# Kernel optimization log

Hardware: AMD Instinct MI355X
Metric: run time of the kernel (lower is better)

Reference implementation:

```python
import jax, jax.numpy as jnp
import numpy as np

HID = 32
R = 3
B = 2
IN = 64
N = 100000
E = 1600000
G = 256


def setup_inputs() -> dict:
    key = jax.random.key(0)
    ks = jax.random.split(key, 16)
    x = jax.random.normal(ks[0], (N, IN), dtype=jnp.float32)
    src = jax.random.randint(ks[1], (E,), 0, N)
    dst = jax.random.randint(ks[2], (E,), 0, N)
    etype = jax.random.randint(ks[3], (E,), 0, R)
    graph_ids = jnp.sort(jax.random.randint(ks[4], (N,), 0, G))
    s = 0.05
    basis1 = jax.random.normal(ks[5], (B, IN, HID), dtype=jnp.float32) * s   # layer 1 basis
    basis_r = jax.random.normal(ks[6], (3, B, HID, HID), dtype=jnp.float32) * s  # layers 2-4
    w_comp = jax.random.normal(ks[7], (4, R, B), dtype=jnp.float32) * s     # per-layer basis coeffs
    loop1 = jax.random.normal(ks[8], (IN, HID), dtype=jnp.float32) * s
    loop_r = jax.random.normal(ks[9], (3, HID, HID), dtype=jnp.float32) * s
    bias = jnp.zeros((4, HID), dtype=jnp.float32)
    lin1_w = jax.random.normal(ks[10], (4 * HID, 64), dtype=jnp.float32) * s
    lin1_b = jnp.zeros((64,), dtype=jnp.float32)
    lin2_w = jax.random.normal(ks[11], (64, 1), dtype=jnp.float32) * s
    lin2_b = jnp.zeros((1,), dtype=jnp.float32)
    return dict(x=x, basis1=basis1, basis_r=basis_r, w_comp=w_comp, loop1=loop1,
                loop_r=loop_r, bias=bias, lin1_w=lin1_w, lin1_b=lin1_b,
                lin2_w=lin2_w, lin2_b=lin2_b, src=src, dst=dst, etype=etype,
                graph_ids=graph_ids, num_graphs=G)


def _rel_conv(h, basis, comp, loop_w, b, src, dst, etype, n_nodes):
    # basis-decomposed relation weights: W[r] = sum_b comp[r,b] * basis[b]
    W = jnp.einsum('rb,bio->rio', comp, basis)            # [R, in, out]
    h_rel = jnp.einsum('ni,rio->rno', h, W)               # [R, N, out]
    msg = h_rel[etype, src]                               # [E, out] edge-typed gather
    agg = jax.ops.segment_sum(msg, dst, num_segments=n_nodes)
    return agg + h @ loop_w + b                           # self-loop + bias


def reference(x, basis1, basis_r, w_comp, loop1, loop_r, bias,
              lin1_w, lin1_b, lin2_w, lin2_b,
              src, dst, etype, graph_ids, num_graphs):
    n = x.shape[0]
    h = jnp.tanh(_rel_conv(x, basis1, w_comp[0], loop1, bias[0], src, dst, etype, n))
    states = [h]
    for i in range(3):
        h = jnp.tanh(_rel_conv(h, basis_r[i], w_comp[i + 1], loop_r[i], bias[i + 1],
                               src, dst, etype, n))
        states.append(h)
    feat = jnp.concatenate(states, axis=1)                # [N, 128]
    # mean-pool nodes per graph (diff_pooling ~ dgl mean_nodes)
    summed = jax.ops.segment_sum(feat, graph_ids, num_segments=num_graphs)
    counts = jax.ops.segment_sum(jnp.ones((n,), feat.dtype), graph_ids,
                                 num_segments=num_graphs)
    pooled = summed / jnp.maximum(counts, 1.0)[:, None]   # [G, 128]
    hdn = jax.nn.relu(pooled @ lin1_w + lin1_b)
    out = jax.nn.sigmoid(hdn @ lin2_w + lin2_b)
    return out[:, 0]
```

## Files before the change

kernel.cpp:

```cpp
#include <hip/hip_runtime.h>
#include <cstdint>
#include <cmath>

#define DLO_BITS 7
#define DLO_MASK 127
#define SCAT_Q 2048

__global__ __launch_bounds__(256) void count_kernel(
    const int* __restrict__ dst, int* __restrict__ bcnt, int E, int NB)
{
    __shared__ int cnt[1024];
    for (int i = threadIdx.x; i < NB; i += 256) cnt[i] = 0;
    __syncthreads();
    int base = blockIdx.x * SCAT_Q;
    #pragma unroll
    for (int i = 0; i < SCAT_Q / 256; ++i) {
        int e = base + i * 256 + threadIdx.x;
        if (e < E) atomicAdd(&cnt[dst[e] >> DLO_BITS], 1);
    }
    __syncthreads();
    for (int i = threadIdx.x; i < NB; i += 256)
        if (cnt[i]) atomicAdd(&bcnt[i], cnt[i]);
}

__global__ __launch_bounds__(1024) void scan_kernel(
    const int* __restrict__ bcnt, int* __restrict__ bbase,
    int* __restrict__ bcur, int NB)
{
    __shared__ int s[1024];
    int t = threadIdx.x;
    int v = (t < NB) ? bcnt[t] : 0;
    s[t] = v; __syncthreads();
    for (int off = 1; off < 1024; off <<= 1) {
        int u = (t >= off) ? s[t - off] : 0;
        __syncthreads();
        s[t] += u;
        __syncthreads();
    }
    if (t < NB) { int b = s[t] - v; bbase[t] = b; bcur[t] = b; }
}

__global__ __launch_bounds__(256) void bscatter_kernel(
    const int* __restrict__ src, const int* __restrict__ dst,
    const int* __restrict__ et, int* __restrict__ bcur,
    unsigned* __restrict__ eidx1, int E, int NB)
{
    __shared__ int cnt[1024];
    __shared__ int bbs[1024];
    int tid = threadIdx.x;
    for (int i = tid; i < NB; i += 256) cnt[i] = 0;
    __syncthreads();
    int base = blockIdx.x * SCAT_Q;
    int lim = E - base; if (lim > SCAT_Q) lim = SCAT_Q;
    for (int i = tid; i < lim; i += 256)
        atomicAdd(&cnt[dst[base + i] >> DLO_BITS], 1);
    __syncthreads();
    for (int i = tid; i < NB; i += 256) {
        int c = cnt[i];
        bbs[i] = c ? atomicAdd(&bcur[i], c) : 0;
    }
    __syncthreads();
    for (int i = tid; i < NB; i += 256) cnt[i] = 0;
    __syncthreads();
    for (int i = tid; i < lim; i += 256) {
        int e = base + i;
        int d = dst[e];
        int bk = d >> DLO_BITS;
        int p = bbs[bk] + atomicAdd(&cnt[bk], 1);
        eidx1[p] = (unsigned)src[e] | ((unsigned)et[e] << 17)
                 | ((unsigned)(d & DLO_MASK) << 19);
    }
}

__global__ __launch_bounds__(256) void bucket_sort_kernel(
    const unsigned* __restrict__ eidx1, const int* __restrict__ bbase,
    const int* __restrict__ bcnt, unsigned* __restrict__ eidx2,
    int* __restrict__ rp, int* __restrict__ rend, int N)
{
    __shared__ int c128[128], excl[128], w[128];
    int tid = threadIdx.x, b = blockIdx.x;
    int gbase = bbase[b], cnt = bcnt[b], n0 = b << DLO_BITS;
    if (tid < 128) c128[tid] = 0;
    __syncthreads();
    for (int k = tid; k < cnt; k += 256)
        atomicAdd(&c128[(eidx1[gbase + k] >> 19) & DLO_MASK], 1);
    __syncthreads();
    if (tid < 128) w[tid] = c128[tid];
    __syncthreads();
    for (int off = 1; off < 128; off <<= 1) {
        int u = (tid < 128 && tid >= off) ? w[tid - off] : 0;
        __syncthreads();
        if (tid < 128) w[tid] += u;
        __syncthreads();
    }
    if (tid < 128) {
        excl[tid] = w[tid] - c128[tid];
        int n = n0 + tid;
        if (n < N) { rp[n] = gbase + excl[tid]; rend[n] = gbase + excl[tid] + c128[tid]; }
        c128[tid] = 0;
    }
    __syncthreads();
    for (int k = tid; k < cnt; k += 256) {
        unsigned pk = eidx1[gbase + k];
        int dlo = (pk >> 19) & DLO_MASK;
        int p = excl[dlo] + atomicAdd(&c128[dlo], 1);
        eidx2[gbase + p] = pk;
    }
}

__global__ __launch_bounds__(256) void dense_kernel(
    const float* __restrict__ x,
    const float* __restrict__ basis1,
    const float* __restrict__ loop1,
    const float* __restrict__ w_comp,
    const float* __restrict__ bias_l,
    float* __restrict__ hrel,
    float* __restrict__ agg,
    int N)
{
    __shared__ float sW[4 * 2048];
    __shared__ float sH[64 * 68];
    const int tid = threadIdx.x;
    for (int i = tid; i < 4 * 2048; i += 256) {
        int m = i >> 11, io = i & 2047;
        float v;
        if (m < 3) v = w_comp[m * 2] * basis1[io] + w_comp[m * 2 + 1] * basis1[2048 + io];
        else       v = loop1[io];
        sW[i] = v;
    }
    const int nb = blockIdx.x * 64;
    for (int idx = tid; idx < 64 * 64; idx += 256) {
        int n = idx >> 6, i = idx & 63;
        int gn = nb + n;
        sH[n * 68 + i] = (gn < N) ? x[(size_t)gn * 64 + i] : 0.0f;
    }
    __syncthreads();

    const int m  = tid >> 6;
    const int l  = tid & 63;
    const int ow = l & 7;
    const int ng = l >> 3;

    float acc[8][4];
    #pragma unroll
    for (int j = 0; j < 8; ++j)
        #pragma unroll
        for (int k = 0; k < 4; ++k) acc[j][k] = 0.0f;

    const float* wb = &sW[m * 2048 + ow * 4];
    #pragma unroll 2
    for (int i = 0; i < 64; i += 4) {
        float4 wv0 = *(const float4*)(wb + (i + 0) * 32);
        float4 wv1 = *(const float4*)(wb + (i + 1) * 32);
        float4 wv2 = *(const float4*)(wb + (i + 2) * 32);
        float4 wv3 = *(const float4*)(wb + (i + 3) * 32);
        #pragma unroll
        for (int j = 0; j < 8; ++j) {
            float4 hv = *(const float4*)&sH[(j * 8 + ng) * 68 + i];
            acc[j][0] += hv.x * wv0.x + hv.y * wv1.x + hv.z * wv2.x + hv.w * wv3.x;
            acc[j][1] += hv.x * wv0.y + hv.y * wv1.y + hv.z * wv2.y + hv.w * wv3.y;
            acc[j][2] += hv.x * wv0.z + hv.y * wv1.z + hv.z * wv2.z + hv.w * wv3.z;
            acc[j][3] += hv.x * wv0.w + hv.y * wv1.w + hv.z * wv2.w + hv.w * wv3.w;
        }
    }

    if (m < 3) {
        #pragma unroll
        for (int j = 0; j < 8; ++j) {
            int n = nb + j * 8 + ng;
            if (n < N)
                *(float4*)&hrel[((size_t)m * N + n) * 32 + ow * 4] =
                    make_float4(acc[j][0], acc[j][1], acc[j][2], acc[j][3]);
        }
    } else {
        float4 bb = *(const float4*)&bias_l[ow * 4];
        #pragma unroll
        for (int j = 0; j < 8; ++j) {
            int n = nb + j * 8 + ng;
            if (n < N)
                *(float4*)&agg[(size_t)n * 32 + ow * 4] =
                    make_float4(acc[j][0] + bb.x, acc[j][1] + bb.y,
                                acc[j][2] + bb.z, acc[j][3] + bb.w);
        }
    }
}

__global__ __launch_bounds__(256) void gather1_kernel(
    const unsigned* __restrict__ eidx, const int* __restrict__ rp,
    const int* __restrict__ rend, const float* __restrict__ hrel,
    const float* __restrict__ agg, float* __restrict__ feat, int N)
{
    int tid = blockIdx.x * 256 + threadIdx.x;
    int n = tid >> 3;
    if (n >= N) return;
    int c = (tid & 7) << 2;
    int base = rp[n], cnt = rend[n] - base;
    const float4 bv = *(const float4*)&agg[(size_t)n * 32 + c];
    float a0[4] = {bv.x, bv.y, bv.z, bv.w};
    float a1[4] = {0, 0, 0, 0}, a2[4] = {0, 0, 0, 0}, a3[4] = {0, 0, 0, 0};
    int k = 0;
    for (; k + 4 <= cnt; k += 4) {
        unsigned p0 = eidx[base + k + 0], p1 = eidx[base + k + 1];
        unsigned p2 = eidx[base + k + 2], p3 = eidx[base + k + 3];
        float4 v0 = *(const float4*)&hrel[(((size_t)((p0 >> 17) & 3)) * N + (p0 & 0x1FFFF)) * 32 + c];
        float4 v1 = *(const float4*)&hrel[(((size_t)((p1 >> 17) & 3)) * N + (p1 & 0x1FFFF)) * 32 + c];
        float4 v2 = *(const float4*)&hrel[(((size_t)((p2 >> 17) & 3)) * N + (p2 & 0x1FFFF)) * 32 + c];
        float4 v3 = *(const float4*)&hrel[(((size_t)((p3 >> 17) & 3)) * N + (p3 & 0x1FFFF)) * 32 + c];
        a0[0] += v0.x; a0[1] += v0.y; a0[2] += v0.z; a0[3] += v0.w;
        a1[0] += v1.x; a1[1] += v1.y; a1[2] += v1.z; a1[3] += v1.w;
        a2[0] += v2.x; a2[1] += v2.y; a2[2] += v2.z; a2[3] += v2.w;
        a3[0] += v3.x; a3[1] += v3.y; a3[2] += v3.z; a3[3] += v3.w;
    }
    for (; k < cnt; ++k) {
        unsigned p = eidx[base + k];
        float4 v = *(const float4*)&hrel[(((size_t)((p >> 17) & 3)) * N + (p & 0x1FFFF)) * 32 + c];
        a0[0] += v.x; a0[1] += v.y; a0[2] += v.z; a0[3] += v.w;
    }
    float r0 = a0[0] + a1[0] + a2[0] + a3[0];
    float r1 = a0[1] + a1[1] + a2[1] + a3[1];
    float r2 = a0[2] + a1[2] + a2[2] + a3[2];
    float r3 = a0[3] + a1[3] + a2[3] + a3[3];
    float4* out = (float4*)&feat[(size_t)n * 128 + c];
    *out = make_float4(tanhf(r0), tanhf(r1), tanhf(r2), tanhf(r3));
}

__global__ __launch_bounds__(256) void fused_layer_kernel(
    const unsigned* __restrict__ eidx, const int* __restrict__ rp,
    const int* __restrict__ rend,
    const float* __restrict__ basis_b,
    const float* __restrict__ loop_w,
    const float* __restrict__ bias_l,
    const float* __restrict__ comp,
    const float* __restrict__ feat_in,
    float* __restrict__ feat_out,
    int N)
{
    __shared__ float sB0[1024], sB1[1024], sL[1024];
    __shared__ float sT0[32 * 36], sT1[32 * 36], sH[32 * 36];
    const int tid = threadIdx.x;
    for (int i = tid; i < 1024; i += 256) {
        sB0[i] = basis_b[i];
        sB1[i] = basis_b[1024 + i];
        sL[i]  = loop_w[i];
    }
    const float cc0r0 = comp[0], cc1r0 = comp[1];
    const float cc0r1 = comp[2], cc1r1 = comp[3];
    const float cc0r2 = comp[4], cc1r2 = comp[5];

    const int nn = tid >> 3, cg = (tid & 7) << 2;
    const int n = blockIdx.x * 32 + nn;

    float4 h4 = *(const float4*)&feat_in[(size_t)n * 128 + cg];
    *(float4*)&sH[nn * 36 + cg] = h4;

    const int base = rp[n], cnt = rend[n] - base;
    float t0a[4] = {0,0,0,0}, t1a[4] = {0,0,0,0};
    float t0b[4] = {0,0,0,0}, t1b[4] = {0,0,0,0};
    int k = 0;
    for (; k + 4 <= cnt; k += 4) {
        unsigned p0 = eidx[base + k + 0], p1 = eidx[base + k + 1];
        unsigned p2 = eidx[base + k + 2], p3 = eidx[base + k + 3];
        int r0 = (p0 >> 17) & 3, r1 = (p1 >> 17) & 3;
        int r2 = (p2 >> 17) & 3, r3 = (p3 >> 17) & 3;
        float4 v0 = *(const float4*)&feat_in[(size_t)(p0 & 0x1FFFF) * 128 + cg];
        float4 v1 = *(const float4*)&feat_in[(size_t)(p1 & 0x1FFFF) * 128 + cg];
        float4 v2 = *(const float4*)&feat_in[(size_t)(p2 & 0x1FFFF) * 128 + cg];
        float4 v3 = *(const float4*)&feat_in[(size_t)(p3 & 0x1FFFF) * 128 + cg];
        float c00 = r0 == 0 ? cc0r0 : (r0 == 1 ? cc0r1 : cc0r2);
        float c10 = r0 == 0 ? cc1r0 : (r0 == 1 ? cc1r1 : cc1r2);
        float c01 = r1 == 0 ? cc0r0 : (r1 == 1 ? cc0r1 : cc0r2);
        float c11 = r1 == 0 ? cc1r0 : (r1 == 1 ? cc1r1 : cc1r2);
        float c02 = r2 == 0 ? cc0r0 : (r2 == 1 ? cc0r1 : cc0r2);
        float c12 = r2 == 0 ? cc1r0 : (r2 == 1 ? cc1r1 : cc1r2);
        float c03 = r3 == 0 ? cc0r0 : (r3 == 1 ? cc0r1 : cc0r2);
        float c13 = r3 == 0 ? cc1r0 : (r3 == 1 ? cc1r1 : cc1r2);
        t0a[0] += c00*v0.x; t0a[1] += c00*v0.y; t0a[2] += c00*v0.z; t0a[3] += c00*v0.w;
        t1a[0] += c10*v0.x; t1a[1] += c10*v0.y; t1a[2] += c10*v0.z; t1a[3] += c10*v0.w;
        t0b[0] += c01*v1.x; t0b[1] += c01*v1.y; t0b[2] += c01*v1.z; t0b[3] += c01*v1.w;
        t1b[0] += c11*v1.x; t1b[1] += c11*v1.y; t1b[2] += c11*v1.z; t1b[3] += c11*v1.w;
        t0a[0] += c02*v2.x; t0a[1] += c02*v2.y; t0a[2] += c02*v2.z; t0a[3] += c02*v2.w;
        t1a[0] += c12*v2.x; t1a[1] += c12*v2.y; t1a[2] += c12*v2.z; t1a[3] += c12*v2.w;
        t0b[0] += c03*v3.x; t0b[1] += c03*v3.y; t0b[2] += c03*v3.z; t0b[3] += c03*v3.w;
        t1b[0] += c13*v3.x; t1b[1] += c13*v3.y; t1b[2] += c13*v3.z; t1b[3] += c13*v3.w;
    }
    for (; k < cnt; ++k) {
        unsigned p = eidx[base + k];
        int r = (p >> 17) & 3;
        float4 v = *(const float4*)&feat_in[(size_t)(p & 0x1FFFF) * 128 + cg];
        float c0 = r == 0 ? cc0r0 : (r == 1 ? cc0r1 : cc0r2);
        float c1 = r == 0 ? cc1r0 : (r == 1 ? cc1r1 : cc1r2);
        t0a[0] += c0*v.x; t0a[1] += c0*v.y; t0a[2] += c0*v.z; t0a[3] += c0*v.w;
        t1a[0] += c1*v.x; t1a[1] += c1*v.y; t1a[2] += c1*v.z; t1a[3] += c1*v.w;
    }
    *(float4*)&sT0[nn * 36 + cg] = make_float4(t0a[0]+t0b[0], t0a[1]+t0b[1],
                                               t0a[2]+t0b[2], t0a[3]+t0b[3]);
    *(float4*)&sT1[nn * 36 + cg] = make_float4(t1a[0]+t1b[0], t1a[1]+t1b[1],
                                               t1a[2]+t1b[2], t1a[3]+t1b[3]);
    __syncthreads();

    float4 bb = *(const float4*)&bias_l[cg];
    float a[4] = {bb.x, bb.y, bb.z, bb.w};
    #pragma unroll 8
    for (int kk = 0; kk < 32; ++kk) {
        float p0 = sT0[nn * 36 + kk];
        float p1 = sT1[nn * 36 + kk];
        float hh = sH[nn * 36 + kk];
        float4 b0 = *(const float4*)&sB0[kk * 32 + cg];
        float4 b1 = *(const float4*)&sB1[kk * 32 + cg];
        float4 lw = *(const float4*)&sL[kk * 32 + cg];
        a[0] += p0 * b0.x + p1 * b1.x + hh * lw.x;
        a[1] += p0 * b0.y + p1 * b1.y + hh * lw.y;
        a[2] += p0 * b0.z + p1 * b1.z + hh * lw.z;
        a[3] += p0 * b0.w + p1 * b1.w + hh * lw.w;
    }
    *(float4*)&feat_out[(size_t)n * 128 + cg] =
        make_float4(tanhf(a[0]), tanhf(a[1]), tanhf(a[2]), tanhf(a[3]));
}

__global__ __launch_bounds__(256) void pool_kernel(
    const float* __restrict__ feat, const int* __restrict__ gid,
    float* __restrict__ pooled, float* __restrict__ cntArr, int N)
{
    int chunk0 = blockIdx.x * 128;
    int ch = threadIdx.x & 127, half = threadIdx.x >> 7;
    int n = chunk0 + half;
    int lim = chunk0 + 128; if (lim > N) lim = N;
    if (n >= lim) return;
    int cur = gid[n];
    float acc = 0.0f; int cc = 0;
    for (; n < lim; n += 2) {
        int g = gid[n];
        if (g != cur) {
            atomicAdd(&pooled[(size_t)cur * 128 + ch], acc);
            if (ch == 0) atomicAdd(&cntArr[cur], (float)cc);
            acc = 0.0f; cc = 0; cur = g;
        }
        acc += feat[(size_t)n * 128 + ch];
        ++cc;
    }
    atomicAdd(&pooled[(size_t)cur * 128 + ch], acc);
    if (ch == 0) atomicAdd(&cntArr[cur], (float)cc);
}

__global__ __launch_bounds__(64) void mlp_kernel(
    const float* __restrict__ pooled, const float* __restrict__ cntArr,
    const float* __restrict__ w1, const float* __restrict__ b1,
    const float* __restrict__ w2, const float* __restrict__ b2,
    float* __restrict__ out)
{
    int g = blockIdx.x;
    int t = threadIdx.x;
    float inv = 1.0f / fmaxf(cntArr[g], 1.0f);
    float acc = b1[t];
    #pragma unroll 8
    for (int k = 0; k < 128; ++k)
        acc += pooled[(size_t)g * 128 + k] * inv * w1[k * 64 + t];
    float h = fmaxf(acc, 0.0f);
    float p = h * w2[t];
    #pragma unroll
    for (int off = 32; off > 0; off >>= 1) p += __shfl_down(p, off, 64);
    if (t == 0) out[g] = 1.0f / (1.0f + expf(-(p + b2[0])));
}

extern "C" void kernel_launch(void* const* d_in, const int* in_sizes, int n_in,
                              void* d_out, int out_size, void* d_ws, size_t ws_size,
                              hipStream_t stream)
{
    const float* x       = (const float*)d_in[0];
    const float* basis1  = (const float*)d_in[1];
    const float* basis_r = (const float*)d_in[2];
    const float* w_comp  = (const float*)d_in[3];
    const float* loop1   = (const float*)d_in[4];
    const float* loop_r  = (const float*)d_in[5];
    const float* bias    = (const float*)d_in[6];
    const float* lin1_w  = (const float*)d_in[7];
    const float* lin1_b  = (const float*)d_in[8];
    const float* lin2_w  = (const float*)d_in[9];
    const float* lin2_b  = (const float*)d_in[10];
    const int*   src     = (const int*)d_in[11];
    const int*   dst     = (const int*)d_in[12];
    const int*   etype   = (const int*)d_in[13];
    const int*   gid     = (const int*)d_in[14];

    const int N = in_sizes[0] / 64;
    const int E = in_sizes[11];
    const int G = out_size;
    const int NB = (N + DLO_MASK) >> DLO_BITS;

    float* ws      = (float*)d_ws;
    float* hrel    = ws;
    float* agg     = hrel + (size_t)3 * N * 32;
    float* feat    = agg + (size_t)N * 32;
    float* pooled  = feat + (size_t)N * 128;
    float* cntArr  = pooled + (size_t)G * 128;
    int*   bcnt    = (int*)(cntArr + G);
    int*   bbase   = bcnt + NB;
    int*   bcur    = bbase + NB;
    int*   rp      = bcur + NB;
    int*   rend    = rp + N;
    unsigned* eidx2 = (unsigned*)(rend + N);
    unsigned* eidx1 = (unsigned*)feat;

    hipMemsetAsync(pooled, 0, ((size_t)G * 128 + G + NB) * sizeof(float), stream);

    const int nsb = (E + SCAT_Q - 1) / SCAT_Q;
    count_kernel<<<nsb, 256, 0, stream>>>(dst, bcnt, E, NB);
    scan_kernel<<<1, 1024, 0, stream>>>(bcnt, bbase, bcur, NB);
    bscatter_kernel<<<nsb, 256, 0, stream>>>(src, dst, etype, bcur, eidx1, E, NB);
    bucket_sort_kernel<<<NB, 256, 0, stream>>>(eidx1, bbase, bcnt, eidx2, rp, rend, N);

    dense_kernel<<<(N + 63) / 64, 256, 0, stream>>>(x, basis1, loop1, w_comp, bias, hrel, agg, N);
    gather1_kernel<<<(N * 8 + 255) / 256, 256, 0, stream>>>(eidx2, rp, rend, hrel, agg, feat, N);

    for (int l = 1; l < 4; ++l) {
        fused_layer_kernel<<<(N + 31) / 32, 256, 0, stream>>>(
            eidx2, rp, rend,
            basis_r + (size_t)(l - 1) * 2048,
            loop_r + (size_t)(l - 1) * 1024,
            bias + l * 32,
            w_comp + l * 6,
            feat + (l - 1) * 32,
            feat + l * 32,
            N);
    }

    pool_kernel<<<(N + 127) / 128, 256, 0, stream>>>(feat, gid, pooled, cntArr, N);
    mlp_kernel<<<G, 64, 0, stream>>>(pooled, cntArr, lin1_w, lin1_b, lin2_w, lin2_b, (float*)d_out);
}
```

Before: 343.7 us.

## Precompute layer-1 relation weights once and read them as wave-uniform scalars in dense kernel

Adds a small prep kernel that builds the combined layer-1 relation and self-loop weights into workspace once, instead of every block rebuilding 32KB of weights in shared memory. The dense kernel is restructured so each wave takes one weight matrix (made wave-uniform with readfirstlane) and each lane computes all 32 outputs for one node, so the weight reads can become scalar loads. This cuts shared-memory use and per-block setup work. In exchange it needs 32 accumulators per lane, adds a kernel launch, and writes full 128-byte rows per lane, which are less coalesced stores.

```diff
diff --git a/kernel.cpp b/kernel.cpp
--- a/kernel.cpp
+++ b/kernel.cpp
@@ -5,6 +5,21 @@
 #define DLO_BITS 7
 #define DLO_MASK 127
 #define SCAT_Q 2048
+
+__global__ __launch_bounds__(256) void prep_w(
+    const float* __restrict__ basis1,
+    const float* __restrict__ w_comp,
+    const float* __restrict__ loop1,
+    float* __restrict__ W)
+{
+    int tid = blockIdx.x * 256 + threadIdx.x;
+    if (tid < 8192) {
+        int m = tid >> 11, io = tid & 2047;
+        W[tid] = (m < 3)
+            ? w_comp[m * 2] * basis1[io] + w_comp[m * 2 + 1] * basis1[2048 + io]
+            : loop1[io];
+    }
+}
 
 __global__ __launch_bounds__(256) void count_kernel(
     const int* __restrict__ dst, int* __restrict__ bcnt, int E, int NB)
@@ -110,24 +125,14 @@
 
 __global__ __launch_bounds__(256) void dense_kernel(
     const float* __restrict__ x,
-    const float* __restrict__ basis1,
-    const float* __restrict__ loop1,
-    const float* __restrict__ w_comp,
+    const float* __restrict__ W,
     const float* __restrict__ bias_l,
     float* __restrict__ hrel,
     float* __restrict__ agg,
     int N)
 {
-    __shared__ float sW[4 * 2048];
     __shared__ float sH[64 * 68];
     const int tid = threadIdx.x;
-    for (int i = tid; i < 4 * 2048; i += 256) {
-        int m = i >> 11, io = i & 2047;
-        float v;
-        if (m < 3) v = w_comp[m * 2] * basis1[io] + w_comp[m * 2 + 1] * basis1[2048 + io];
-        else       v = loop1[io];
-        sW[i] = v;
-    }
     const int nb = blockIdx.x * 64;
     for (int idx = tid; idx < 64 * 64; idx += 256) {
         int n = idx >> 6, i = idx & 63;
@@ -136,51 +141,37 @@
     }
     __syncthreads();
 
-    const int m  = tid >> 6;
-    const int l  = tid & 63;
-    const int ow = l & 7;
-    const int ng = l >> 3;
-
-    float acc[8][4];
+    const int m = __builtin_amdgcn_readfirstlane(tid >> 6);
+    const int l = tid & 63;
+    const float* wm = W + m * 2048;
+
+    float acc[32];
     #pragma unroll
-    for (int j = 0; j < 8; ++j)
+    for (int c = 0; c < 32; ++c) acc[c] = 0.0f;
+
+    #pragma unroll
+    for (int k0 = 0; k0 < 64; k0 += 4) {
+        float4 xv = *(const float4*)&sH[l * 68 + k0];
+        const float* w0 = wm + k0 * 32;
         #pragma unroll
-        for (int k = 0; k < 4; ++k) acc[j][k] = 0.0f;
-
-    const float* wb = &sW[m * 2048 + ow * 4];
-    #pragma unroll 2
-    for (int i = 0; i < 64; i += 4) {
-        float4 wv0 = *(const float4*)(wb + (i + 0) * 32);
-        float4 wv1 = *(const float4*)(wb + (i + 1) * 32);
-        float4 wv2 = *(const float4*)(wb + (i + 2) * 32);
-        float4 wv3 = *(const float4*)(wb + (i + 3) * 32);
-        #pragma unroll
-        for (int j = 0; j < 8; ++j) {
-            float4 hv = *(const float4*)&sH[(j * 8 + ng) * 68 + i];
-            acc[j][0] += hv.x * wv0.x + hv.y * wv1.x + hv.z * wv2.x + hv.w * wv3.x;
-            acc[j][1] += hv.x * wv0.y + hv.y * wv1.y + hv.z * wv2.y + hv.w * wv3.y;
-            acc[j][2] += hv.x * wv0.z + hv.y * wv1.z + hv.z * wv2.z + hv.w * wv3.z;
-            acc[j][3] += hv.x * wv0.w + hv.y * wv1.w + hv.z * wv2.w + hv.w * wv3.w;
-        }
-    }
-
-    if (m < 3) {
-        #pragma unroll
-        for (int j = 0; j < 8; ++j) {
-            int n = nb + j * 8 + ng;
-            if (n < N)
-                *(float4*)&hrel[((size_t)m * N + n) * 32 + ow * 4] =
-                    make_float4(acc[j][0], acc[j][1], acc[j][2], acc[j][3]);
-        }
-    } else {
-        float4 bb = *(const float4*)&bias_l[ow * 4];
-        #pragma unroll
-        for (int j = 0; j < 8; ++j) {
-            int n = nb + j * 8 + ng;
-            if (n < N)
-                *(float4*)&agg[(size_t)n * 32 + ow * 4] =
-                    make_float4(acc[j][0] + bb.x, acc[j][1] + bb.y,
-                                acc[j][2] + bb.z, acc[j][3] + bb.w);
+        for (int c = 0; c < 32; ++c)
+            acc[c] += xv.x * w0[c] + xv.y * w0[32 + c]
+                    + xv.z * w0[64 + c] + xv.w * w0[96 + c];
+    }
+
+    int n = nb + l;
+    if (n < N) {
+        if (m < 3) {
+            float* out = &hrel[((size_t)m * N + n) * 32];
+            #pragma unroll
+            for (int c = 0; c < 32; c += 4)
+                *(float4*)(out + c) = make_float4(acc[c], acc[c+1], acc[c+2], acc[c+3]);
+        } else {
+            float* out = &agg[(size_t)n * 32];
+            #pragma unroll
+            for (int c = 0; c < 32; c += 4)
+                *(float4*)(out + c) = make_float4(acc[c] + bias_l[c],   acc[c+1] + bias_l[c+1],
+                                                  acc[c+2] + bias_l[c+2], acc[c+3] + bias_l[c+3]);
         }
     }
 }
@@ -388,7 +379,8 @@
     const int NB = (N + DLO_MASK) >> DLO_BITS;
 
     float* ws      = (float*)d_ws;
-    float* hrel    = ws;
+    float* W       = ws;
+    float* hrel    = W + 8192;
     float* agg     = hrel + (size_t)3 * N * 32;
     float* feat    = agg + (size_t)N * 32;
     float* pooled  = feat + (size_t)N * 128;
@@ -402,6 +394,7 @@
     unsigned* eidx1 = (unsigned*)feat;
 
     hipMemsetAsync(pooled, 0, ((size_t)G * 128 + G + NB) * sizeof(float), stream);
+    prep_w<<<32, 256, 0, stream>>>(basis1, w_comp, loop1, W);
 
     const int nsb = (E + SCAT_Q - 1) / SCAT_Q;
     count_kernel<<<nsb, 256, 0, stream>>>(dst, bcnt, E, NB);
@@ -409,7 +402,7 @@
     bscatter_kernel<<<nsb, 256, 0, stream>>>(src, dst, etype, bcur, eidx1, E, NB);
     bucket_sort_kernel<<<NB, 256, 0, stream>>>(eidx1, bbase, bcnt, eidx2, rp, rend, N);
 
-    dense_kernel<<<(N + 63) / 64, 256, 0, stream>>>(x, basis1, loop1, w_comp, bias, hrel, agg, N);
+    dense_kernel<<<(N + 63) / 64, 256, 0, stream>>>(x, W, bias, hrel, agg, N);
     gather1_kernel<<<(N * 8 + 255) / 256, 256, 0, stream>>>(eidx2, rp, rend, hrel, agg, feat, N);
 
     for (int l = 1; l < 4; ++l) {
```

Measured after the change: 347.1 us. Within noise of the previous version (+1.0%).

## Sort edges by (dst, etype) to drop per-edge relation selects in gathers

Applied to the files above, without the earlier changes.

The bucket sort now keys on destination node and edge type together, producing three per-relation segment boundaries per node. Gather kernels loop over each relation segment separately, so the fused layers apply the basis coefficients once per segment instead of selecting and multiplying per edge, and layer 1 uses a fixed relation base pointer. The combined relation weights for layer 1 are also precomputed once in a small kernel instead of being rebuilt in every dense block. In exchange the sort scans 512 keys instead of 128, two extra offset arrays are written and read, and the split loops have shorter unrolled bodies with more tail handling.

```diff
diff --git a/kernel.cpp b/kernel.cpp
--- a/kernel.cpp
+++ b/kernel.cpp
@@ -5,6 +5,21 @@
 #define DLO_BITS 7
 #define DLO_MASK 127
 #define SCAT_Q 2048
+
+__global__ __launch_bounds__(256) void prep_w(
+    const float* __restrict__ basis1,
+    const float* __restrict__ w_comp,
+    const float* __restrict__ loop1,
+    float* __restrict__ W)
+{
+    int tid = blockIdx.x * 256 + threadIdx.x;
+    if (tid < 8192) {
+        int m = tid >> 11, io = tid & 2047;
+        W[tid] = (m < 3)
+            ? w_comp[m * 2] * basis1[io] + w_comp[m * 2 + 1] * basis1[2048 + io]
+            : loop1[io];
+    }
+}
 
 __global__ __launch_bounds__(256) void count_kernel(
     const int* __restrict__ dst, int* __restrict__ bcnt, int E, int NB)
@@ -75,44 +90,56 @@
 __global__ __launch_bounds__(256) void bucket_sort_kernel(
     const unsigned* __restrict__ eidx1, const int* __restrict__ bbase,
     const int* __restrict__ bcnt, unsigned* __restrict__ eidx2,
-    int* __restrict__ rp, int* __restrict__ rend, int N)
-{
-    __shared__ int c128[128], excl[128], w[128];
+    int* __restrict__ rp, int* __restrict__ rend0, int* __restrict__ rend1,
+    int* __restrict__ rend, int N)
+{
+    __shared__ int c512[512], excl[512], w[512];
     int tid = threadIdx.x, b = blockIdx.x;
     int gbase = bbase[b], cnt = bcnt[b], n0 = b << DLO_BITS;
-    if (tid < 128) c128[tid] = 0;
-    __syncthreads();
-    for (int k = tid; k < cnt; k += 256)
-        atomicAdd(&c128[(eidx1[gbase + k] >> 19) & DLO_MASK], 1);
-    __syncthreads();
-    if (tid < 128) w[tid] = c128[tid];
-    __syncthreads();
-    for (int off = 1; off < 128; off <<= 1) {
-        int u = (tid < 128 && tid >= off) ? w[tid - off] : 0;
-        __syncthreads();
-        if (tid < 128) w[tid] += u;
-        __syncthreads();
-    }
-    if (tid < 128) {
-        excl[tid] = w[tid] - c128[tid];
-        int n = n0 + tid;
-        if (n < N) { rp[n] = gbase + excl[tid]; rend[n] = gbase + excl[tid] + c128[tid]; }
-        c128[tid] = 0;
-    }
+    c512[tid] = 0; c512[tid + 256] = 0;
     __syncthreads();
     for (int k = tid; k < cnt; k += 256) {
         unsigned pk = eidx1[gbase + k];
-        int dlo = (pk >> 19) & DLO_MASK;
-        int p = excl[dlo] + atomicAdd(&c128[dlo], 1);
+        int key = (((pk >> 19) & DLO_MASK) << 2) | ((pk >> 17) & 3);
+        atomicAdd(&c512[key], 1);
+    }
+    __syncthreads();
+    w[tid] = c512[tid]; w[tid + 256] = c512[tid + 256];
+    __syncthreads();
+    for (int off = 1; off < 512; off <<= 1) {
+        int a1 = (tid >= off) ? w[tid - off] : 0;
+        int a2 = (tid + 256 >= off) ? w[tid + 256 - off] : 0;
+        __syncthreads();
+        w[tid] += a1; w[tid + 256] += a2;
+        __syncthreads();
+    }
+    excl[tid] = w[tid] - c512[tid];
+    excl[tid + 256] = w[tid + 256] - c512[tid + 256];
+    __syncthreads();
+    if (tid < 128) {
+        int n = n0 + tid;
+        if (n < N) {
+            int k0 = tid << 2;
+            rp[n]    = gbase + excl[k0];
+            rend0[n] = gbase + excl[k0 | 1];
+            rend1[n] = gbase + excl[k0 | 2];
+            rend[n]  = gbase + excl[k0 | 2] + c512[k0 | 2];
+        }
+    }
+    __syncthreads();
+    c512[tid] = 0; c512[tid + 256] = 0;
+    __syncthreads();
+    for (int k = tid; k < cnt; k += 256) {
+        unsigned pk = eidx1[gbase + k];
+        int key = (((pk >> 19) & DLO_MASK) << 2) | ((pk >> 17) & 3);
+        int p = excl[key] + atomicAdd(&c512[key], 1);
         eidx2[gbase + p] = pk;
     }
 }
 
 __global__ __launch_bounds__(256) void dense_kernel(
     const float* __restrict__ x,
-    const float* __restrict__ basis1,
-    const float* __restrict__ loop1,
-    const float* __restrict__ w_comp,
+    const float* __restrict__ W,
     const float* __restrict__ bias_l,
     float* __restrict__ hrel,
     float* __restrict__ agg,
@@ -121,13 +148,7 @@
     __shared__ float sW[4 * 2048];
     __shared__ float sH[64 * 68];
     const int tid = threadIdx.x;
-    for (int i = tid; i < 4 * 2048; i += 256) {
-        int m = i >> 11, io = i & 2047;
-        float v;
-        if (m < 3) v = w_comp[m * 2] * basis1[io] + w_comp[m * 2 + 1] * basis1[2048 + io];
-        else       v = loop1[io];
-        sW[i] = v;
-    }
+    for (int i = tid; i < 4 * 2048; i += 256) sW[i] = W[i];
     const int nb = blockIdx.x * 64;
     for (int idx = tid; idx < 64 * 64; idx += 256) {
         int n = idx >> 6, i = idx & 63;
@@ -187,45 +208,45 @@
 
 __global__ __launch_bounds__(256) void gather1_kernel(
     const unsigned* __restrict__ eidx, const int* __restrict__ rp,
-    const int* __restrict__ rend, const float* __restrict__ hrel,
-    const float* __restrict__ agg, float* __restrict__ feat, int N)
+    const int* __restrict__ rend0, const int* __restrict__ rend1,
+    const int* __restrict__ rend,
+    const float* __restrict__ hrel, const float* __restrict__ agg,
+    float* __restrict__ feat, int N)
 {
     int tid = blockIdx.x * 256 + threadIdx.x;
     int n = tid >> 3;
     if (n >= N) return;
     int c = (tid & 7) << 2;
-    int base = rp[n], cnt = rend[n] - base;
+    int e0 = rp[n], e1 = rend0[n], e2 = rend1[n], e3 = rend[n];
     const float4 bv = *(const float4*)&agg[(size_t)n * 32 + c];
-    float a0[4] = {bv.x, bv.y, bv.z, bv.w};
-    float a1[4] = {0, 0, 0, 0}, a2[4] = {0, 0, 0, 0}, a3[4] = {0, 0, 0, 0};
-    int k = 0;
-    for (; k + 4 <= cnt; k += 4) {
-        unsigned p0 = eidx[base + k + 0], p1 = eidx[base + k + 1];
-        unsigned p2 = eidx[base + k + 2], p3 = eidx[base + k + 3];
-        float4 v0 = *(const float4*)&hrel[(((size_t)((p0 >> 17) & 3)) * N + (p0 & 0x1FFFF)) * 32 + c];
-        float4 v1 = *(const float4*)&hrel[(((size_t)((p1 >> 17) & 3)) * N + (p1 & 0x1FFFF)) * 32 + c];
-        float4 v2 = *(const float4*)&hrel[(((size_t)((p2 >> 17) & 3)) * N + (p2 & 0x1FFFF)) * 32 + c];
-        float4 v3 = *(const float4*)&hrel[(((size_t)((p3 >> 17) & 3)) * N + (p3 & 0x1FFFF)) * 32 + c];
-        a0[0] += v0.x; a0[1] += v0.y; a0[2] += v0.z; a0[3] += v0.w;
-        a1[0] += v1.x; a1[1] += v1.y; a1[2] += v1.z; a1[3] += v1.w;
-        a2[0] += v2.x; a2[1] += v2.y; a2[2] += v2.z; a2[3] += v2.w;
-        a3[0] += v3.x; a3[1] += v3.y; a3[2] += v3.z; a3[3] += v3.w;
-    }
-    for (; k < cnt; ++k) {
-        unsigned p = eidx[base + k];
-        float4 v = *(const float4*)&hrel[(((size_t)((p >> 17) & 3)) * N + (p & 0x1FFFF)) * 32 + c];
-        a0[0] += v.x; a0[1] += v.y; a0[2] += v.z; a0[3] += v.w;
-    }
-    float r0 = a0[0] + a1[0] + a2[0] + a3[0];
-    float r1 = a0[1] + a1[1] + a2[1] + a3[1];
-    float r2 = a0[2] + a1[2] + a2[2] + a3[2];
-    float r3 = a0[3] + a1[3] + a2[3] + a3[3];
+    float ax = bv.x, ay = bv.y, az = bv.z, aw = bv.w;
+    float bx = 0, by = 0, bz = 0, bw = 0;
+    #pragma unroll
+    for (int seg = 0; seg < 3; ++seg) {
+        int ks = (seg == 0) ? e0 : ((seg == 1) ? e1 : e2);
+        int ke = (seg == 0) ? e1 : ((seg == 1) ? e2 : e3);
+        const float* hb = hrel + (size_t)seg * N * 32 + c;
+        int k = ks;
+        for (; k + 2 <= ke; k += 2) {
+            unsigned p0 = eidx[k], p1 = eidx[k + 1];
+            float4 v0 = *(const float4*)&hb[(size_t)(p0 & 0x1FFFF) * 32];
+            float4 v1 = *(const float4*)&hb[(size_t)(p1 & 0x1FFFF) * 32];
+            ax += v0.x; ay += v0.y; az += v0.z; aw += v0.w;
+            bx += v1.x; by += v1.y; bz += v1.z; bw += v1.w;
+        }
+        if (k < ke) {
+            unsigned p = eidx[k];
+            float4 v = *(const float4*)&hb[(size_t)(p & 0x1FFFF) * 32];
+            ax += v.x; ay += v.y; az += v.z; aw += v.w;
+        }
+    }
     float4* out = (float4*)&feat[(size_t)n * 128 + c];
-    *out = make_float4(tanhf(r0), tanhf(r1), tanhf(r2), tanhf(r3));
+    *out = make_float4(tanhf(ax + bx), tanhf(ay + by), tanhf(az + bz), tanhf(aw + bw));
 }
 
 __global__ __launch_bounds__(256) void fused_layer_kernel(
     const unsigned* __restrict__ eidx, const int* __restrict__ rp,
+    const int* __restrict__ rend0, const int* __restrict__ rend1,
     const int* __restrict__ rend,
     const float* __restrict__ basis_b,
     const float* __restrict__ loop_w,
@@ -243,59 +264,41 @@
         sB1[i] = basis_b[1024 + i];
         sL[i]  = loop_w[i];
     }
-    const float cc0r0 = comp[0], cc1r0 = comp[1];
-    const float cc0r1 = comp[2], cc1r1 = comp[3];
-    const float cc0r2 = comp[4], cc1r2 = comp[5];
-
     const int nn = tid >> 3, cg = (tid & 7) << 2;
     const int n = blockIdx.x * 32 + nn;
 
     float4 h4 = *(const float4*)&feat_in[(size_t)n * 128 + cg];
     *(float4*)&sH[nn * 36 + cg] = h4;
 
-    const int base = rp[n], cnt = rend[n] - base;
-    float t0a[4] = {0,0,0,0}, t1a[4] = {0,0,0,0};
-    float t0b[4] = {0,0,0,0}, t1b[4] = {0,0,0,0};
-    int k = 0;
-    for (; k + 4 <= cnt; k += 4) {
-        unsigned p0 = eidx[base + k + 0], p1 = eidx[base + k + 1];
-        unsigned p2 = eidx[base + k + 2], p3 = eidx[base + k + 3];
-        int r0 = (p0 >> 17) & 3, r1 = (p1 >> 17) & 3;
-        int r2 = (p2 >> 17) & 3, r3 = (p3 >> 17) & 3;
-        float4 v0 = *(const float4*)&feat_in[(size_t)(p0 & 0x1FFFF) * 128 + cg];
-        float4 v1 = *(const float4*)&feat_in[(size_t)(p1 & 0x1FFFF) * 128 + cg];
-        float4 v2 = *(const float4*)&feat_in[(size_t)(p2 & 0x1FFFF) * 128 + cg];
-        float4 v3 = *(const float4*)&feat_in[(size_t)(p3 & 0x1FFFF) * 128 + cg];
-        float c00 = r0 == 0 ? cc0r0 : (r0 == 1 ? cc0r1 : cc0r2);
-        float c10 = r0 == 0 ? cc1r0 : (r0 == 1 ? cc1r1 : cc1r2);
-        float c01 = r1 == 0 ? cc0r0 : (r1 == 1 ? cc0r1 : cc0r2);
-        float c11 = r1 == 0 ? cc1r0 : (r1 == 1 ? cc1r1 : cc1r2);
-        float c02 = r2 == 0 ? cc0r0 : (r2 == 1 ? cc0r1 : cc0r2);
-        float c12 = r2 == 0 ? cc1r0 : (r2 == 1 ? cc1r1 : cc1r2);
-        float c03 = r3 == 0 ? cc0r0 : (r3 == 1 ? cc0r1 : cc0r2);
-        float c13 = r3 == 0 ? cc1r0 : (r3 == 1 ? cc1r1 : cc1r2);
-        t0a[0] += c00*v0.x; t0a[1] += c00*v0.y; t0a[2] += c00*v0.z; t0a[3] += c00*v0.w;
-        t1a[0] += c10*v0.x; t1a[1] += c10*v0.y; t1a[2] += c10*v0.z; t1a[3] += c10*v0.w;
-        t0b[0] += c01*v1.x; t0b[1] += c01*v1.y; t0b[2] += c01*v1.z; t0b[3] += c01*v1.w;
-        t1b[0] += c11*v1.x; t1b[1] += c11*v1.y; t1b[2] += c11*v1.z; t1b[3] += c11*v1.w;
-        t0a[0] += c02*v2.x; t0a[1] += c02*v2.y; t0a[2] += c02*v2.z; t0a[3] += c02*v2.w;
-        t1a[0] += c12*v2.x; t1a[1] += c12*v2.y; t1a[2] += c12*v2.z; t1a[3] += c12*v2.w;
-        t0b[0] += c03*v3.x; t0b[1] += c03*v3.y; t0b[2] += c03*v3.z; t0b[3] += c03*v3.w;
-        t1b[0] += c13*v3.x; t1b[1] += c13*v3.y; t1b[2] += c13*v3.z; t1b[3] += c13*v3.w;
-    }
-    for (; k < cnt; ++k) {
-        unsigned p = eidx[base + k];
-        int r = (p >> 17) & 3;
-        float4 v = *(const float4*)&feat_in[(size_t)(p & 0x1FFFF) * 128 + cg];
-        float c0 = r == 0 ? cc0r0 : (r == 1 ? cc0r1 : cc0r2);
-        float c1 = r == 0 ? cc1r0 : (r == 1 ? cc1r1 : cc1r2);
-        t0a[0] += c0*v.x; t0a[1] += c0*v.y; t0a[2] += c0*v.z; t0a[3] += c0*v.w;
-        t1a[0] += c1*v.x; t1a[1] += c1*v.y; t1a[2] += c1*v.z; t1a[3] += c1*v.w;
-    }
-    *(float4*)&sT0[nn * 36 + cg] = make_float4(t0a[0]+t0b[0], t0a[1]+t0b[1],
-                                               t0a[2]+t0b[2], t0a[3]+t0b[3]);
-    *(float4*)&sT1[nn * 36 + cg] = make_float4(t1a[0]+t1b[0], t1a[1]+t1b[1],
-                                               t1a[2]+t1b[2], t1a[3]+t1b[3]);
+    int e0 = rp[n], e1 = rend0[n], e2 = rend1[n], e3 = rend[n];
+    float t0x = 0, t0y = 0, t0z = 0, t0w = 0;
+    float t1x = 0, t1y = 0, t1z = 0, t1w = 0;
+    #pragma unroll
+    for (int seg = 0; seg < 3; ++seg) {
+        int ks = (seg == 0) ? e0 : ((seg == 1) ? e1 : e2);
+        int ke = (seg == 0) ? e1 : ((seg == 1) ? e2 : e3);
+        float sx = 0, sy = 0, sz = 0, sw = 0;
+        float ux = 0, uy = 0, uz = 0, uw = 0;
+        int k = ks;
+        for (; k + 2 <= ke; k += 2) {
+            unsigned p0 = eidx[k], p1 = eidx[k + 1];
+            float4 v0 = *(const float4*)&feat_in[(size_t)(p0 & 0x1FFFF) * 128 + cg];
+            float4 v1 = *(const float4*)&feat_in[(size_t)(p1 & 0x1FFFF) * 128 + cg];
+            sx += v0.x; sy += v0.y; sz += v0.z; sw += v0.w;
+            ux += v1.x; uy += v1.y; uz += v1.z; uw += v1.w;
+        }
+        if (k < ke) {
+            unsigned p = eidx[k];
+            float4 v = *(const float4*)&feat_in[(size_t)(p & 0x1FFFF) * 128 + cg];
+            sx += v.x; sy += v.y; sz += v.z; sw += v.w;
+        }
+        sx += ux; sy += uy; sz += uz; sw += uw;
+        float c0 = comp[seg * 2], c1 = comp[seg * 2 + 1];
+        t0x += c0 * sx; t0y += c0 * sy; t0z += c0 * sz; t0w += c0 * sw;
+        t1x += c1 * sx; t1y += c1 * sy; t1z += c1 * sz; t1w += c1 * sw;
+    }
+    *(float4*)&sT0[nn * 36 + cg] = make_float4(t0x, t0y, t0z, t0w);
+    *(float4*)&sT1[nn * 36 + cg] = make_float4(t1x, t1y, t1z, t1w);
     __syncthreads();
 
     float4 bb = *(const float4*)&bias_l[cg];
@@ -388,7 +391,8 @@
     const int NB = (N + DLO_MASK) >> DLO_BITS;
 
     float* ws      = (float*)d_ws;
-    float* hrel    = ws;
+    float* W       = ws;
+    float* hrel    = W + 8192;
     float* agg     = hrel + (size_t)3 * N * 32;
     float* feat    = agg + (size_t)N * 32;
     float* pooled  = feat + (size_t)N * 128;
@@ -397,24 +401,29 @@
     int*   bbase   = bcnt + NB;
     int*   bcur    = bbase + NB;
     int*   rp      = bcur + NB;
-    int*   rend    = rp + N;
+    int*   rend0   = rp + N;
+    int*   rend1   = rend0 + N;
+    int*   rend    = rend1 + N;
     unsigned* eidx2 = (unsigned*)(rend + N);
     unsigned* eidx1 = (unsigned*)feat;
 
     hipMemsetAsync(pooled, 0, ((size_t)G * 128 + G + NB) * sizeof(float), stream);
+    prep_w<<<32, 256, 0, stream>>>(basis1, w_comp, loop1, W);
 
     const int nsb = (E + SCAT_Q - 1) / SCAT_Q;
     count_kernel<<<nsb, 256, 0, stream>>>(dst, bcnt, E, NB);
     scan_kernel<<<1, 1024, 0, stream>>>(bcnt, bbase, bcur, NB);
     bscatter_kernel<<<nsb, 256, 0, stream>>>(src, dst, etype, bcur, eidx1, E, NB);
-    bucket_sort_kernel<<<NB, 256, 0, stream>>>(eidx1, bbase, bcnt, eidx2, rp, rend, N);
-
-    dense_kernel<<<(N + 63) / 64, 256, 0, stream>>>(x, basis1, loop1, w_comp, bias, hrel, agg, N);
-    gather1_kernel<<<(N * 8 + 255) / 256, 256, 0, stream>>>(eidx2, rp, rend, hrel, agg, feat, N);
+    bucket_sort_kernel<<<NB, 256, 0, stream>>>(eidx1, bbase, bcnt, eidx2,
+                                               rp, rend0, rend1, rend, N);
+
+    dense_kernel<<<(N + 63) / 64, 256, 0, stream>>>(x, W, bias, hrel, agg, N);
+    gather1_kernel<<<(N * 8 + 255) / 256, 256, 0, stream>>>(
+        eidx2, rp, rend0, rend1, rend, hrel, agg, feat, N);
 
     for (int l = 1; l < 4; ++l) {
         fused_layer_kernel<<<(N + 31) / 32, 256, 0, stream>>>(
-            eidx2, rp, rend,
+            eidx2, rp, rend0, rend1, rend,
             basis_r + (size_t)(l - 1) * 2048,
             loop_r + (size_t)(l - 1) * 1024,
             bias + l * 32,
```

New measurement: 360.0 us. 4.7% more time.
